# Kernel optimization log

Measured on AMD Instinct MI355X. Metric: run time of the kernel, lower is better.

## Reference

```python
import jax, jax.numpy as jnp
import numpy as np

EPS = 1e-6

def absmean_quantize(W):
    # gamma = mean |W| + eps; quantize to {-1,0,1}
    gamma = jnp.abs(W).mean() + EPS
    Ws = W / gamma
    return jnp.sign(Ws) * jnp.minimum(jnp.round(jnp.abs(Ws)), 1.0)

def setup_inputs() -> dict:
    key = jax.random.key(0)
    k1, k2 = jax.random.split(key)
    B, S, D_IN, D_OUT = 4, 2048, 4096, 16384
    x = jax.random.normal(k1, (B, S, D_IN), dtype=jnp.float32)
    weight = jax.random.normal(k2, (D_OUT, D_IN), dtype=jnp.float32)
    return {"x": x, "weight": weight}

def reference(x, weight):
    # BitLinear158 forward: ternary-quantize weight, then linear (no bias)
    qw = absmean_quantize(weight)  # [out, in]
    return jnp.einsum('bsi,oi->bso', x, qw)
```

## Files before the change

### kernel.cpp

```cpp
#include <hip/hip_runtime.h>
#include <hip/hip_bf16.h>
#include <stdint.h>

typedef unsigned short u16;
typedef __bf16 bf16x8 __attribute__((ext_vector_type(8)));
typedef float f32x4 __attribute__((ext_vector_type(4)));

#define M_DIM 8192
#define N_DIM 16384
#define K_DIM 4096

#define BM 128
#define BN 128
#define BK 64

struct alignas(8) us4 { u16 x, y, z, w; };

__device__ __forceinline__ void gload_lds16(const u16* g, u16* l) {
  __builtin_amdgcn_global_load_lds((const __attribute__((address_space(1))) void*)g,
                                   (__attribute__((address_space(3))) void*)l,
                                   16, 0, 0);
}

__device__ __forceinline__ u16 f32_to_bf16_rne_bits(float f) {
  uint32_t b = __float_as_uint(f);
  uint32_t r = b + 0x7FFFu + ((b >> 16) & 1u);
  return (u16)(r >> 16);
}

__global__ __launch_bounds__(256) void absum_kernel(const float* __restrict__ W,
                                                    double* __restrict__ out, int n4) {
  int tid = blockIdx.x * blockDim.x + threadIdx.x;
  int stride = gridDim.x * blockDim.x;
  const float4* W4 = (const float4*)W;
  double s = 0.0;
  for (int i = tid; i < n4; i += stride) {
    float4 v = W4[i];
    s += (double)fabsf(v.x) + (double)fabsf(v.y) +
         (double)fabsf(v.z) + (double)fabsf(v.w);
  }
  for (int off = 32; off > 0; off >>= 1)
    s += __shfl_down(s, off, 64);
  __shared__ double wsum[4];
  int l = threadIdx.x & 63, w = threadIdx.x >> 6;
  if (l == 0) wsum[w] = s;
  __syncthreads();
  if (threadIdx.x == 0) {
    double t = wsum[0] + wsum[1] + wsum[2] + wsum[3];
    atomicAdd(out, t);
  }
}

__global__ __launch_bounds__(256) void quant_kernel(const float* __restrict__ W,
                                                    const double* __restrict__ gsum,
                                                    u16* __restrict__ Bq, int n4) {
  float gamma = (float)(*gsum * (1.0 / (double)((size_t)N_DIM * K_DIM))) + 1e-6f;
  int tid = blockIdx.x * blockDim.x + threadIdx.x;
  int stride = gridDim.x * blockDim.x;
  const float4* W4 = (const float4*)W;
  us4* B4 = (us4*)Bq;
  for (int i = tid; i < n4; i += stride) {
    float4 v = W4[i];
    float q0 = copysignf(fminf(rintf(fabsf(v.x / gamma)), 1.0f), v.x);
    float q1 = copysignf(fminf(rintf(fabsf(v.y / gamma)), 1.0f), v.y);
    float q2 = copysignf(fminf(rintf(fabsf(v.z / gamma)), 1.0f), v.z);
    float q3 = copysignf(fminf(rintf(fabsf(v.w / gamma)), 1.0f), v.w);
    us4 o;
    o.x = (u16)(__float_as_uint(q0) >> 16);
    o.y = (u16)(__float_as_uint(q1) >> 16);
    o.z = (u16)(__float_as_uint(q2) >> 16);
    o.w = (u16)(__float_as_uint(q3) >> 16);
    B4[i] = o;
  }
}

__global__ __launch_bounds__(256) void split_kernel(const float* __restrict__ x,
                                                    u16* __restrict__ hi,
                                                    u16* __restrict__ lo, int n4) {
  int tid = blockIdx.x * blockDim.x + threadIdx.x;
  int stride = gridDim.x * blockDim.x;
  const float4* X4 = (const float4*)x;
  us4* H4 = (us4*)hi;
  us4* L4 = (us4*)lo;
  for (int i = tid; i < n4; i += stride) {
    float4 v = X4[i];
    us4 h, l;
    h.x = f32_to_bf16_rne_bits(v.x);
    h.y = f32_to_bf16_rne_bits(v.y);
    h.z = f32_to_bf16_rne_bits(v.z);
    h.w = f32_to_bf16_rne_bits(v.w);
    l.x = f32_to_bf16_rne_bits(v.x - __uint_as_float((uint32_t)h.x << 16));
    l.y = f32_to_bf16_rne_bits(v.y - __uint_as_float((uint32_t)h.y << 16));
    l.z = f32_to_bf16_rne_bits(v.z - __uint_as_float((uint32_t)h.z << 16));
    l.w = f32_to_bf16_rne_bits(v.w - __uint_as_float((uint32_t)h.w << 16));
    H4[i] = h;
    L4[i] = l;
  }
}

__global__ __launch_bounds__(256, 3) void gemm_kernel(const u16* __restrict__ Ahi,
                                                      const u16* __restrict__ Alo,
                                                      const u16* __restrict__ Bq,
                                                      float* __restrict__ C) {
  __shared__ __align__(16) u16 lAhi[BM * BK];
  __shared__ __align__(16) u16 lAlo[BM * BK];
  __shared__ __align__(16) u16 lB[BN * BK];

  int wg = blockIdx.x;
  wg = (wg & 7) * 1024 + (wg >> 3);
  const int tm = wg >> 7;
  const int tn = wg & 127;

  const int tid = threadIdx.x;
  const int w = tid >> 6;
  const int l = tid & 63;
  const int wr = w >> 1, wc = w & 1;
  const int lr = l & 15;
  const int lk = (l >> 4) * 8;

  const int rbase = tid >> 3;
  const int cbase = (tid & 7) * 8;
  const u16* pAhi = Ahi + (size_t)(tm * BM + rbase) * K_DIM + cbase;
  const u16* pAlo = Alo + (size_t)(tm * BM + rbase) * K_DIM + cbase;
  const u16* pB   = Bq  + (size_t)(tn * BN + rbase) * K_DIM + cbase;

  f32x4 acc[4][4];
#pragma unroll
  for (int i = 0; i < 4; ++i)
#pragma unroll
    for (int j = 0; j < 4; ++j)
      acc[i][j] = (f32x4){0.f, 0.f, 0.f, 0.f};

  for (int k0 = 0; k0 < K_DIM; k0 += BK) {
#pragma unroll
    for (int i = 0; i < 4; ++i) {
      gload_lds16(pAhi + (size_t)(i * 32) * K_DIM + k0, &lAhi[i * 2048 + w * 512]);
      gload_lds16(pAlo + (size_t)(i * 32) * K_DIM + k0, &lAlo[i * 2048 + w * 512]);
      gload_lds16(pB   + (size_t)(i * 32) * K_DIM + k0, &lB  [i * 2048 + w * 512]);
    }
    __syncthreads();

#pragma unroll
    for (int kk = 0; kk < 2; ++kk) {
      bf16x8 b[4];
#pragma unroll
      for (int n = 0; n < 4; ++n)
        b[n] = *(const bf16x8*)&lB[(wc * 64 + n * 16 + lr) * BK + kk * 32 + lk];

      bf16x8 a[4];
#pragma unroll
      for (int m = 0; m < 4; ++m)
        a[m] = *(const bf16x8*)&lAhi[(wr * 64 + m * 16 + lr) * BK + kk * 32 + lk];
#pragma unroll
      for (int n = 0; n < 4; ++n)
#pragma unroll
        for (int m = 0; m < 4; ++m)
          acc[m][n] = __builtin_amdgcn_mfma_f32_16x16x32_bf16(a[m], b[n], acc[m][n], 0, 0, 0);

#pragma unroll
      for (int m = 0; m < 4; ++m)
        a[m] = *(const bf16x8*)&lAlo[(wr * 64 + m * 16 + lr) * BK + kk * 32 + lk];
#pragma unroll
      for (int n = 0; n < 4; ++n)
#pragma unroll
        for (int m = 0; m < 4; ++m)
          acc[m][n] = __builtin_amdgcn_mfma_f32_16x16x32_bf16(a[m], b[n], acc[m][n], 0, 0, 0);
    }
    __syncthreads();
  }

#pragma unroll
  for (int m = 0; m < 4; ++m) {
    int row = tm * BM + wr * 64 + m * 16 + (l >> 4) * 4;
#pragma unroll
    for (int n = 0; n < 4; ++n) {
      int col = tn * BN + wc * 64 + n * 16 + lr;
      float* cp = C + (size_t)row * N_DIM + col;
#pragma unroll
      for (int j = 0; j < 4; ++j)
        cp[(size_t)j * N_DIM] = acc[m][n][j];
    }
  }
}

extern "C" void kernel_launch(void* const* d_in, const int* in_sizes, int n_in,
                              void* d_out, int out_size, void* d_ws, size_t ws_size,
                              hipStream_t stream) {
  const float* x = (const float*)d_in[0];
  const float* W = (const float*)d_in[1];
  float* C = (float*)d_out;

  double* gsum = (double*)d_ws;
  u16* Ahi = (u16*)((char*)d_ws + 256);
  u16* Alo = Ahi + (size_t)M_DIM * K_DIM;
  u16* Bq  = Alo + (size_t)M_DIM * K_DIM;

  hipMemsetAsync(d_ws, 0, 8, stream);
  absum_kernel<<<dim3(2048), dim3(256), 0, stream>>>(W, gsum, (N_DIM * K_DIM) / 4);
  quant_kernel<<<dim3(2048), dim3(256), 0, stream>>>(W, gsum, Bq, (N_DIM * K_DIM) / 4);
  split_kernel<<<dim3(2048), dim3(256), 0, stream>>>(x, Ahi, Alo, (M_DIM * K_DIM) / 4);
  gemm_kernel<<<dim3((M_DIM / BM) * (N_DIM / BN)), dim3(256), 0, stream>>>(Ahi, Alo, Bq, C);
}
```

Baseline: 2.579 ms.

## Switch GEMM to int8 MFMA with fixed-point hi/lo split of activations

```diff
diff --git a/kernel.cpp b/kernel.cpp
--- a/kernel.cpp
+++ b/kernel.cpp
@@ -1,10 +1,7 @@
 #include <hip/hip_runtime.h>
-#include <hip/hip_bf16.h>
 #include <stdint.h>
 
-typedef unsigned short u16;
-typedef __bf16 bf16x8 __attribute__((ext_vector_type(8)));
-typedef float f32x4 __attribute__((ext_vector_type(4)));
+typedef int i32x4 __attribute__((ext_vector_type(4)));
 
 #define M_DIM 8192
 #define N_DIM 16384
@@ -14,97 +11,106 @@
 #define BN 128
 #define BK 64
 
-struct alignas(8) us4 { u16 x, y, z, w; };
-
-__device__ __forceinline__ void gload_lds16(const u16* g, u16* l) {
+__device__ __forceinline__ void gload_lds16(const void* g, void* l) {
   __builtin_amdgcn_global_load_lds((const __attribute__((address_space(1))) void*)g,
                                    (__attribute__((address_space(3))) void*)l,
                                    16, 0, 0);
 }
 
-__device__ __forceinline__ u16 f32_to_bf16_rne_bits(float f) {
-  uint32_t b = __float_as_uint(f);
-  uint32_t r = b + 0x7FFFu + ((b >> 16) & 1u);
-  return (u16)(r >> 16);
-}
-
-__global__ __launch_bounds__(256) void absum_kernel(const float* __restrict__ W,
-                                                    double* __restrict__ out, int n4) {
+__global__ __launch_bounds__(256) void reduce_kernel(const float* __restrict__ W,
+                                                     const float* __restrict__ x,
+                                                     double* __restrict__ gsum,
+                                                     unsigned* __restrict__ xmax,
+                                                     int nW4, int nX4) {
   int tid = blockIdx.x * blockDim.x + threadIdx.x;
   int stride = gridDim.x * blockDim.x;
   const float4* W4 = (const float4*)W;
+  const float4* X4 = (const float4*)x;
   double s = 0.0;
-  for (int i = tid; i < n4; i += stride) {
+  for (int i = tid; i < nW4; i += stride) {
     float4 v = W4[i];
     s += (double)fabsf(v.x) + (double)fabsf(v.y) +
          (double)fabsf(v.z) + (double)fabsf(v.w);
   }
-  for (int off = 32; off > 0; off >>= 1)
+  float m = 0.f;
+  for (int i = tid; i < nX4; i += stride) {
+    float4 v = X4[i];
+    m = fmaxf(m, fmaxf(fmaxf(fabsf(v.x), fabsf(v.y)), fmaxf(fabsf(v.z), fabsf(v.w))));
+  }
+  for (int off = 32; off > 0; off >>= 1) {
     s += __shfl_down(s, off, 64);
+    m = fmaxf(m, __shfl_down(m, off, 64));
+  }
   __shared__ double wsum[4];
+  __shared__ float wmax[4];
   int l = threadIdx.x & 63, w = threadIdx.x >> 6;
-  if (l == 0) wsum[w] = s;
+  if (l == 0) { wsum[w] = s; wmax[w] = m; }
   __syncthreads();
   if (threadIdx.x == 0) {
-    double t = wsum[0] + wsum[1] + wsum[2] + wsum[3];
-    atomicAdd(out, t);
+    atomicAdd(gsum, wsum[0] + wsum[1] + wsum[2] + wsum[3]);
+    float mm = fmaxf(fmaxf(wmax[0], wmax[1]), fmaxf(wmax[2], wmax[3]));
+    atomicMax(xmax, __float_as_uint(mm));
   }
 }
 
 __global__ __launch_bounds__(256) void quant_kernel(const float* __restrict__ W,
                                                     const double* __restrict__ gsum,
-                                                    u16* __restrict__ Bq, int n4) {
+                                                    char* __restrict__ Bq, int n4) {
   float gamma = (float)(*gsum * (1.0 / (double)((size_t)N_DIM * K_DIM))) + 1e-6f;
   int tid = blockIdx.x * blockDim.x + threadIdx.x;
   int stride = gridDim.x * blockDim.x;
   const float4* W4 = (const float4*)W;
-  us4* B4 = (us4*)Bq;
+  char4* B4 = (char4*)Bq;
   for (int i = tid; i < n4; i += stride) {
     float4 v = W4[i];
     float q0 = copysignf(fminf(rintf(fabsf(v.x / gamma)), 1.0f), v.x);
     float q1 = copysignf(fminf(rintf(fabsf(v.y / gamma)), 1.0f), v.y);
     float q2 = copysignf(fminf(rintf(fabsf(v.z / gamma)), 1.0f), v.z);
     float q3 = copysignf(fminf(rintf(fabsf(v.w / gamma)), 1.0f), v.w);
-    us4 o;
-    o.x = (u16)(__float_as_uint(q0) >> 16);
-    o.y = (u16)(__float_as_uint(q1) >> 16);
-    o.z = (u16)(__float_as_uint(q2) >> 16);
-    o.w = (u16)(__float_as_uint(q3) >> 16);
+    char4 o;
+    o.x = (char)(int)q0; o.y = (char)(int)q1;
+    o.z = (char)(int)q2; o.w = (char)(int)q3;
     B4[i] = o;
   }
 }
 
 __global__ __launch_bounds__(256) void split_kernel(const float* __restrict__ x,
-                                                    u16* __restrict__ hi,
-                                                    u16* __restrict__ lo, int n4) {
+                                                    const unsigned* __restrict__ xmax,
+                                                    char* __restrict__ hi,
+                                                    char* __restrict__ lo, int n4) {
+  float amax = __uint_as_float(*xmax);
+  float inv = 32512.f / (amax + 1e-30f);
   int tid = blockIdx.x * blockDim.x + threadIdx.x;
   int stride = gridDim.x * blockDim.x;
   const float4* X4 = (const float4*)x;
-  us4* H4 = (us4*)hi;
-  us4* L4 = (us4*)lo;
+  char4* H4 = (char4*)hi;
+  char4* L4 = (char4*)lo;
   for (int i = tid; i < n4; i += stride) {
     float4 v = X4[i];
-    us4 h, l;
-    h.x = f32_to_bf16_rne_bits(v.x);
-    h.y = f32_to_bf16_rne_bits(v.y);
-    h.z = f32_to_bf16_rne_bits(v.z);
-    h.w = f32_to_bf16_rne_bits(v.w);
-    l.x = f32_to_bf16_rne_bits(v.x - __uint_as_float((uint32_t)h.x << 16));
-    l.y = f32_to_bf16_rne_bits(v.y - __uint_as_float((uint32_t)h.y << 16));
-    l.z = f32_to_bf16_rne_bits(v.z - __uint_as_float((uint32_t)h.z << 16));
-    l.w = f32_to_bf16_rne_bits(v.w - __uint_as_float((uint32_t)h.w << 16));
+    float q[4] = {v.x, v.y, v.z, v.w};
+    char hh[4], ll[4];
+#pragma unroll
+    for (int j = 0; j < 4; ++j) {
+      float qf = fminf(fmaxf(rintf(q[j] * inv), -32512.f), 32512.f);
+      float hf = rintf(qf * (1.f / 256.f));
+      float lf = qf - 256.f * hf;
+      if (lf > 127.f) { hf += 1.f; lf -= 256.f; }
+      hh[j] = (char)(int)hf;
+      ll[j] = (char)(int)lf;
+    }
+    char4 h = {hh[0], hh[1], hh[2], hh[3]};
+    char4 l = {ll[0], ll[1], ll[2], ll[3]};
     H4[i] = h;
     L4[i] = l;
   }
 }
 
-__global__ __launch_bounds__(256, 3) void gemm_kernel(const u16* __restrict__ Ahi,
-                                                      const u16* __restrict__ Alo,
-                                                      const u16* __restrict__ Bq,
+__global__ __launch_bounds__(512, 4) void gemm_kernel(const char* __restrict__ Ahi,
+                                                      const char* __restrict__ Alo,
+                                                      const char* __restrict__ Bq,
+                                                      const unsigned* __restrict__ xmax,
                                                       float* __restrict__ C) {
-  __shared__ __align__(16) u16 lAhi[BM * BK];
-  __shared__ __align__(16) u16 lAlo[BM * BK];
-  __shared__ __align__(16) u16 lB[BN * BK];
+  __shared__ __align__(16) char lds[24576];
 
   int wg = blockIdx.x;
   wg = (wg & 7) * 1024 + (wg >> 3);
@@ -114,71 +120,66 @@
   const int tid = threadIdx.x;
   const int w = tid >> 6;
   const int l = tid & 63;
-  const int wr = w >> 1, wc = w & 1;
-  const int lr = l & 15;
-  const int lk = (l >> 4) * 8;
-
-  const int rbase = tid >> 3;
-  const int cbase = (tid & 7) * 8;
-  const u16* pAhi = Ahi + (size_t)(tm * BM + rbase) * K_DIM + cbase;
-  const u16* pAlo = Alo + (size_t)(tm * BM + rbase) * K_DIM + cbase;
-  const u16* pB   = Bq  + (size_t)(tn * BN + rbase) * K_DIM + cbase;
-
-  f32x4 acc[4][4];
-#pragma unroll
-  for (int i = 0; i < 4; ++i)
-#pragma unroll
-    for (int j = 0; j < 4; ++j)
-      acc[i][j] = (f32x4){0.f, 0.f, 0.f, 0.f};
+  const int wr = w >> 2;
+  const int wc = w & 3;
+  const int lr15 = l & 15;
+  const int lk16 = (l >> 4) << 4;
+
+  const char* srcs[3];
+  const char* dsts[3];
+#pragma unroll
+  for (int j = 0; j < 3; ++j) {
+    int job = w * 3 + j;
+    const char* base = (job < 8) ? Ahi : (job < 16) ? Alo : Bq;
+    int s = job & 7;
+    int rowb = (job < 16) ? tm * BM : tn * BN;
+    srcs[j] = base + (size_t)(rowb + s * 16 + lr15) * K_DIM + lk16;
+    dsts[j] = &lds[job * 1024];
+  }
+
+  i32x4 acch[4][2], accl[4][2];
+#pragma unroll
+  for (int m = 0; m < 4; ++m)
+#pragma unroll
+    for (int n = 0; n < 2; ++n) {
+      acch[m][n] = (i32x4){0, 0, 0, 0};
+      accl[m][n] = (i32x4){0, 0, 0, 0};
+    }
 
   for (int k0 = 0; k0 < K_DIM; k0 += BK) {
 #pragma unroll
-    for (int i = 0; i < 4; ++i) {
-      gload_lds16(pAhi + (size_t)(i * 32) * K_DIM + k0, &lAhi[i * 2048 + w * 512]);
-      gload_lds16(pAlo + (size_t)(i * 32) * K_DIM + k0, &lAlo[i * 2048 + w * 512]);
-      gload_lds16(pB   + (size_t)(i * 32) * K_DIM + k0, &lB  [i * 2048 + w * 512]);
-    }
+    for (int j = 0; j < 3; ++j)
+      gload_lds16(srcs[j] + k0, (void*)(dsts[j]));
     __syncthreads();
 
-#pragma unroll
-    for (int kk = 0; kk < 2; ++kk) {
-      bf16x8 b[4];
-#pragma unroll
-      for (int n = 0; n < 4; ++n)
-        b[n] = *(const bf16x8*)&lB[(wc * 64 + n * 16 + lr) * BK + kk * 32 + lk];
-
-      bf16x8 a[4];
-#pragma unroll
-      for (int m = 0; m < 4; ++m)
-        a[m] = *(const bf16x8*)&lAhi[(wr * 64 + m * 16 + lr) * BK + kk * 32 + lk];
-#pragma unroll
-      for (int n = 0; n < 4; ++n)
-#pragma unroll
-        for (int m = 0; m < 4; ++m)
-          acc[m][n] = __builtin_amdgcn_mfma_f32_16x16x32_bf16(a[m], b[n], acc[m][n], 0, 0, 0);
-
-#pragma unroll
-      for (int m = 0; m < 4; ++m)
-        a[m] = *(const bf16x8*)&lAlo[(wr * 64 + m * 16 + lr) * BK + kk * 32 + lk];
-#pragma unroll
-      for (int n = 0; n < 4; ++n)
-#pragma unroll
-        for (int m = 0; m < 4; ++m)
-          acc[m][n] = __builtin_amdgcn_mfma_f32_16x16x32_bf16(a[m], b[n], acc[m][n], 0, 0, 0);
+    i32x4 b0 = *(const i32x4*)&lds[16384 + (wc * 2 + 0) * 1024 + l * 16];
+    i32x4 b1 = *(const i32x4*)&lds[16384 + (wc * 2 + 1) * 1024 + l * 16];
+#pragma unroll
+    for (int m = 0; m < 4; ++m) {
+      i32x4 a = *(const i32x4*)&lds[(wr * 4 + m) * 1024 + l * 16];
+      acch[m][0] = __builtin_amdgcn_mfma_i32_16x16x64_i8(a, b0, acch[m][0], 0, 0, 0);
+      acch[m][1] = __builtin_amdgcn_mfma_i32_16x16x64_i8(a, b1, acch[m][1], 0, 0, 0);
+    }
+#pragma unroll
+    for (int m = 0; m < 4; ++m) {
+      i32x4 a = *(const i32x4*)&lds[8192 + (wr * 4 + m) * 1024 + l * 16];
+      accl[m][0] = __builtin_amdgcn_mfma_i32_16x16x64_i8(a, b0, accl[m][0], 0, 0, 0);
+      accl[m][1] = __builtin_amdgcn_mfma_i32_16x16x64_i8(a, b1, accl[m][1], 0, 0, 0);
     }
     __syncthreads();
   }
 
+  const float sc = __uint_as_float(*xmax) * (1.f / 32512.f);
 #pragma unroll
   for (int m = 0; m < 4; ++m) {
     int row = tm * BM + wr * 64 + m * 16 + (l >> 4) * 4;
 #pragma unroll
-    for (int n = 0; n < 4; ++n) {
-      int col = tn * BN + wc * 64 + n * 16 + lr;
+    for (int n = 0; n < 2; ++n) {
+      int col = tn * BN + wc * 32 + n * 16 + lr15;
       float* cp = C + (size_t)row * N_DIM + col;
 #pragma unroll
       for (int j = 0; j < 4; ++j)
-        cp[(size_t)j * N_DIM] = acc[m][n][j];
+        cp[(size_t)j * N_DIM] = sc * fmaf(256.f, (float)acch[m][n][j], (float)accl[m][n][j]);
     }
   }
 }
@@ -191,13 +192,16 @@
   float* C = (float*)d_out;
 
   double* gsum = (double*)d_ws;
-  u16* Ahi = (u16*)((char*)d_ws + 256);
-  u16* Alo = Ahi + (size_t)M_DIM * K_DIM;
-  u16* Bq  = Alo + (size_t)M_DIM * K_DIM;
-
-  hipMemsetAsync(d_ws, 0, 8, stream);
-  absum_kernel<<<dim3(2048), dim3(256), 0, stream>>>(W, gsum, (N_DIM * K_DIM) / 4);
+  unsigned* xmax = (unsigned*)((char*)d_ws + 8);
+  char* Ahi = (char*)d_ws + 256;
+  char* Alo = Ahi + (size_t)M_DIM * K_DIM;
+  char* Bq  = Alo + (size_t)M_DIM * K_DIM;
+
+  hipMemsetAsync(d_ws, 0, 16, stream);
+  reduce_kernel<<<dim3(2048), dim3(256), 0, stream>>>(W, x, gsum, xmax,
+                                                      (N_DIM * K_DIM) / 4,
+                                                      (M_DIM * K_DIM) / 4);
   quant_kernel<<<dim3(2048), dim3(256), 0, stream>>>(W, gsum, Bq, (N_DIM * K_DIM) / 4);
-  split_kernel<<<dim3(2048), dim3(256), 0, stream>>>(x, Ahi, Alo, (M_DIM * K_DIM) / 4);
-  gemm_kernel<<<dim3((M_DIM / BM) * (N_DIM / BN)), dim3(256), 0, stream>>>(Ahi, Alo, Bq, C);
-}
+  split_kernel<<<dim3(2048), dim3(256), 0, stream>>>(x, xmax, Ahi, Alo, (M_DIM * K_DIM) / 4);
+  gemm_kernel<<<dim3((M_DIM / BM) * (N_DIM / BN)), dim3(512), 0, stream>>>(Ahi, Alo, Bq, xmax, C);
+}
```

Result: faster. 2.300 ms (-10.8%).
